# Performance work log

Hardware: AMD Instinct MI355X
Metric: run time of the kernel (lower is better)

The kernel has to match this reference:

```python
import jax, jax.numpy as jnp
import numpy as np

M_LOCAL = 100000
N_GLOBAL = 50000
C = 128
E = 1600000
EDGE_DIM = 16
BN_EPS = 1e-5


def setup_inputs() -> dict:
    key = jax.random.key(0)
    ks = jax.random.split(key, 12)
    s = 1.0 / np.sqrt(C)
    inp = {
        "h_local": jax.random.normal(ks[0], (M_LOCAL, C), jnp.float32),
        "h_global": jax.random.normal(ks[1], (N_GLOBAL, C), jnp.float32),
        "ea_flat": jax.random.normal(ks[2], (E, EDGE_DIM), jnp.float32),
        # GIN MLP: Linear(C,C) -> ReLU -> Linear(C,C)
        "W1": jax.random.normal(ks[3], (C, C), jnp.float32) * s,
        "b1": jnp.zeros((C,), jnp.float32),
        "W2": jax.random.normal(ks[4], (C, C), jnp.float32) * s,
        "b2": jnp.zeros((C,), jnp.float32),
        "eps": jnp.zeros((), jnp.float32),  # GIN train_eps, init 0
        "gamma_l": jnp.ones((C,), jnp.float32),
        "beta_l": jnp.zeros((C,), jnp.float32),
        "gamma_g": jnp.ones((C,), jnp.float32),
        "beta_g": jnp.zeros((C,), jnp.float32),
        "intra_ei": jax.random.randint(ks[5], (2, E), 0, M_LOCAL, jnp.int32),
        "node_ids": jax.random.randint(ks[6], (M_LOCAL,), 0, N_GLOBAL, jnp.int32),
        "valid": jnp.ones((M_LOCAL,), jnp.bool_),
        "N_total": N_GLOBAL,
    }
    return inp


def _batchnorm(x, gamma, beta):
    # training-mode BN: biased batch statistics over node dim
    mu = jnp.mean(x, axis=0)
    var = jnp.mean((x - mu) ** 2, axis=0)
    return (x - mu) * jax.lax.rsqrt(var + BN_EPS) * gamma + beta


def reference(h_local, h_global, ea_flat, W1, b1, W2, b2, eps,
              gamma_l, beta_l, gamma_g, beta_g,
              intra_ei, node_ids, valid, N_total):
    M = h_local.shape[0]
    valid_f = valid.astype(h_local.dtype)[:, None]
    clamped = jnp.maximum(node_ids, 0)

    # inject global context, zero padding
    h_in = (h_local + h_global[clamped]) * valid_f

    # GINConv: mlp((1+eps)*x + sum_{j->i} x_j)   (ea_flat unused for 'gin')
    src, dst = intra_ei[0], intra_ei[1]
    agg = jax.ops.segment_sum(h_in[src], dst, num_segments=M)
    pre = (1.0 + eps) * h_in + agg
    h_local_new = jnp.maximum(pre @ W1 + b1, 0.0) @ W2 + b2
    h_local_new = h_local_new * valid_f

    # cross-subgraph consensus: scatter mean into global nodes
    h_sum = jax.ops.segment_sum(h_local_new, clamped, num_segments=N_total)
    v_cnt = jax.ops.segment_sum(valid_f[:, 0], clamped, num_segments=N_total)
    h_global_new = h_sum / jnp.maximum(v_cnt, 1.0)[:, None]

    # local track: BN + residual (Identity since in==out) + mask (dropout p=0)
    h_local_new = _batchnorm(h_local_new, gamma_l, beta_l) + h_local
    h_local_new = h_local_new * valid_f

    # global track: BN + residual
    h_global_new = _batchnorm(h_global_new, gamma_g, beta_g) + h_global

    return (h_local_new, h_global_new)
```

## Files before the change

kernel.cpp:

```cpp
#include <hip/hip_runtime.h>

#define CDIM 128
#define BROWS 128
#define QROWS 32
#define SMAXQ 1024
#define CHUNK 16384
#define GMB 2048
#define H1LD 136

typedef __bf16 bf16x8 __attribute__((ext_vector_type(8)));
typedef __bf16 bf16x4 __attribute__((ext_vector_type(4)));
typedef float f32x4 __attribute__((ext_vector_type(4)));

__global__ __launch_bounds__(256) void k_init(
    const float* __restrict__ hl, const float* __restrict__ hg,
    const int* __restrict__ nid, __bf16* __restrict__ h_in, int M)
{
    int idx = blockIdx.x * 256 + threadIdx.x;
    if (idx >= M * 16) return;
    int i = idx >> 4, q8 = idx & 15;
    int g = max(nid[i], 0);
    const float4* hl4 = reinterpret_cast<const float4*>(hl);
    const float4* hg4 = reinterpret_cast<const float4*>(hg);
    float4 a0 = hl4[i * 32 + q8 * 2], a1 = hl4[i * 32 + q8 * 2 + 1];
    float4 b0 = hg4[g * 32 + q8 * 2], b1 = hg4[g * 32 + q8 * 2 + 1];
    bf16x8 o;
    o[0] = (__bf16)(a0.x + b0.x); o[1] = (__bf16)(a0.y + b0.y);
    o[2] = (__bf16)(a0.z + b0.z); o[3] = (__bf16)(a0.w + b0.w);
    o[4] = (__bf16)(a1.x + b1.x); o[5] = (__bf16)(a1.y + b1.y);
    o[6] = (__bf16)(a1.z + b1.z); o[7] = (__bf16)(a1.w + b1.w);
    *reinterpret_cast<bf16x8*>(&h_in[(size_t)i * CDIM + q8 * 8]) = o;
}

__global__ __launch_bounds__(256) void k_count(
    const int* __restrict__ ei, const int* __restrict__ nid,
    int* __restrict__ bcnt, int* __restrict__ deg_g, int E, int M)
{
    __shared__ int lh[1024];
    int t = threadIdx.x;
    for (int i = t; i < 1024; i += 256) lh[i] = 0;
    __syncthreads();
    int stride = gridDim.x * 256;
    for (int e = blockIdx.x * 256 + t; e < E; e += stride)
        atomicAdd(&lh[ei[E + e] >> 7], 1);
    for (int i = blockIdx.x * 256 + t; i < M; i += stride)
        atomicAdd(&deg_g[max(nid[i], 0)], 1);
    __syncthreads();
    for (int i = t; i < 1024; i += 256)
        if (lh[i]) atomicAdd(&bcnt[i], lh[i]);
}

__global__ __launch_bounds__(1024) void k_scanA(
    const int* __restrict__ deg_g, int* __restrict__ bsum_g, int N, int nbN,
    const int* __restrict__ bcnt, int* __restrict__ bboff,
    int* __restrict__ bcur, int NB)
{
    __shared__ int sh[1024];
    int t = threadIdx.x;
    if ((int)blockIdx.x < nbN) {
        int i = blockIdx.x * 1024 + t;
        sh[t] = (i < N) ? deg_g[i] : 0;
        __syncthreads();
        for (int s = 512; s > 0; s >>= 1) {
            if (t < s) sh[t] += sh[t + s];
            __syncthreads();
        }
        if (t == 0) bsum_g[blockIdx.x] = sh[0];
    } else {
        int v = (t < NB) ? bcnt[t] : 0;
        sh[t] = v;
        __syncthreads();
        for (int s = 1; s < 1024; s <<= 1) {
            int a = (t >= s) ? sh[t - s] : 0;
            __syncthreads();
            sh[t] += a;
            __syncthreads();
        }
        if (t < NB) { int ex = sh[t] - v; bboff[t] = ex; bcur[t] = ex; }
        if (t == 0) bboff[NB] = sh[1023];
    }
}

__global__ __launch_bounds__(256) void k_scanB(int* __restrict__ bsum, int nb)
{
    __shared__ int sh[256];
    int t = threadIdx.x;
    int v = (t < nb) ? bsum[t] : 0;
    sh[t] = v;
    __syncthreads();
    for (int s = 1; s < 256; s <<= 1) {
        int a = (t >= s) ? sh[t - s] : 0;
        __syncthreads();
        sh[t] += a;
        __syncthreads();
    }
    if (t < nb) bsum[t] = sh[t] - v;
}

__global__ __launch_bounds__(1024) void k_scanC(
    const int* __restrict__ deg_g, const int* __restrict__ bsum_g,
    int* __restrict__ off_g, int N)
{
    __shared__ int sh[1024];
    int i = blockIdx.x * 1024 + threadIdx.x;
    int v = (i < N) ? deg_g[i] : 0;
    sh[threadIdx.x] = v;
    __syncthreads();
    for (int s = 1; s < 1024; s <<= 1) {
        int a = (threadIdx.x >= (unsigned)s) ? sh[threadIdx.x - s] : 0;
        __syncthreads();
        sh[threadIdx.x] += a;
        __syncthreads();
    }
    if (i < N) off_g[i] = bsum_g[blockIdx.x] + sh[threadIdx.x] - v;
}

__global__ __launch_bounds__(256) void k_bscatter(
    const int* __restrict__ ei, const int* __restrict__ nid,
    int* __restrict__ bcur, int* __restrict__ packed,
    const int* __restrict__ off_g, int* __restrict__ cur_g,
    int* __restrict__ rows_g, int E, int M)
{
    __shared__ int lh[1024];
    int t = threadIdx.x;
    int e0 = blockIdx.x * CHUNK;
    int n = min(CHUNK, E - e0);
    for (int i = t; i < 1024; i += 256) lh[i] = 0;
    __syncthreads();
    for (int j = t; j < n; j += 256)
        atomicAdd(&lh[ei[E + e0 + j] >> 7], 1);
    __syncthreads();
    for (int i = t; i < 1024; i += 256) {
        int c = lh[i];
        if (c) lh[i] = atomicAdd(&bcur[i], c);
    }
    __syncthreads();
    for (int j = t; j < n; j += 256) {
        int s = ei[e0 + j], d = ei[E + e0 + j];
        int pos = atomicAdd(&lh[d >> 7], 1);
        packed[pos] = s | ((d & 127) << 17);
    }
    for (int i = blockIdx.x * 256 + t; i < M; i += gridDim.x * 256) {
        int g = max(nid[i], 0);
        int pos = off_g[g] + atomicAdd(&cur_g[g], 1);
        rows_g[pos] = i;
    }
}

__global__ __launch_bounds__(256) void k_agg_fused(
    const __bf16* __restrict__ h_in, const int* __restrict__ packed,
    const int* __restrict__ bboff, const float* __restrict__ epsp,
    __bf16* __restrict__ pre, int M)
{
    __shared__ int lsrc[SMAXQ];
    __shared__ int lcnt[QROWS], lbase[QROWS], lpos[QROWS];
    int t = threadIdx.x;
    int b = blockIdx.x >> 2;
    int quarter = blockIdx.x & 3;
    int base = bboff[b];
    int n = bboff[b + 1] - base;
    if (t < QROWS) lcnt[t] = 0;
    __syncthreads();
    for (int j = t; j < n; j += 256) {
        int ld = packed[base + j] >> 17;
        if ((ld >> 5) == quarter) atomicAdd(&lcnt[ld & 31], 1);
    }
    __syncthreads();
    int v = (t < QROWS) ? lcnt[t] : 0;
    if (t < QROWS) lbase[t] = v;
    __syncthreads();
    for (int s = 1; s < QROWS; s <<= 1) {
        int a = (t < QROWS && t >= s) ? lbase[t - s] : 0;
        __syncthreads();
        if (t < QROWS) lbase[t] += a;
        __syncthreads();
    }
    if (t < QROWS) { lbase[t] -= v; lpos[t] = lbase[t]; }
    __syncthreads();
    for (int j = t; j < n; j += 256) {
        int p = packed[base + j];
        int ld = p >> 17;
        if ((ld >> 5) == quarter) {
            int r = atomicAdd(&lpos[ld & 31], 1);
            if (r < SMAXQ) lsrc[r] = p & 0x1FFFF;
        }
    }
    __syncthreads();

    float es = 1.0f + epsp[0];
    int slot = t >> 4, q = t & 15;
    int r0 = b * BROWS + quarter * QROWS;
#pragma unroll
    for (int rr0 = 0; rr0 < 2; ++rr0) {
        int rr = slot + rr0 * 16;
        int row = r0 + rr;
        if (row >= M) break;
        bf16x8 a = *reinterpret_cast<const bf16x8*>(&h_in[(size_t)row * CDIM + q * 8]);
        float f[8];
#pragma unroll
        for (int k2 = 0; k2 < 8; ++k2) f[k2] = es * (float)a[k2];
        int sb = lbase[rr], cnt = lcnt[rr];
        int j = 0;
        for (; j + 1 < cnt; j += 2) {
            int s0 = lsrc[sb + j], s1 = lsrc[sb + j + 1];
            bf16x8 v0 = *reinterpret_cast<const bf16x8*>(&h_in[(size_t)s0 * CDIM + q * 8]);
            bf16x8 v1 = *reinterpret_cast<const bf16x8*>(&h_in[(size_t)s1 * CDIM + q * 8]);
#pragma unroll
            for (int k2 = 0; k2 < 8; ++k2) f[k2] += (float)v0[k2] + (float)v1[k2];
        }
        if (j < cnt) {
            int s0 = lsrc[sb + j];
            bf16x8 v0 = *reinterpret_cast<const bf16x8*>(&h_in[(size_t)s0 * CDIM + q * 8]);
#pragma unroll
            for (int k2 = 0; k2 < 8; ++k2) f[k2] += (float)v0[k2];
        }
        bf16x8 o;
#pragma unroll
        for (int k2 = 0; k2 < 8; ++k2) o[k2] = (__bf16)f[k2];
        *reinterpret_cast<bf16x8*>(&pre[(size_t)row * CDIM + q * 8]) = o;
    }
}

__global__ __launch_bounds__(256) void k_wprep(
    const float* __restrict__ W1, const float* __restrict__ W2,
    __bf16* __restrict__ Wt1, __bf16* __restrict__ Wt2)
{
    int idx = blockIdx.x * 256 + threadIdx.x;
    int k = idx >> 7, n = idx & 127;
    Wt1[n * CDIM + k] = (__bf16)W1[k * CDIM + n];
    Wt2[n * CDIM + k] = (__bf16)W2[k * CDIM + n];
}

__global__ __launch_bounds__(256) void k_mlp(
    const __bf16* __restrict__ pre, const __bf16* __restrict__ Wt1,
    const __bf16* __restrict__ Wt2, const float* __restrict__ b1,
    const float* __restrict__ b2, __bf16* __restrict__ y,
    float* __restrict__ part, int M)
{
    __shared__ bf16x8 w_lds4[2048];
    __shared__ __bf16 h1t[64 * H1LD];
    __shared__ float pst[256];
    int t = threadIdx.x;
#pragma unroll
    for (int j = 0; j < 8; ++j) {
        int c = t + j * 256;
        int n = c >> 4, cr = c & 15, kc = cr >> 2, g = cr & 3;
        w_lds4[((n >> 4) * 4 + kc) * 64 + g * 16 + (n & 15)] =
            reinterpret_cast<const bf16x8*>(Wt1)[c];
    }
    if (t < 256) pst[t] = 0.f;
    __syncthreads();

    int wave = t >> 6, lane = t & 63;
    int r0 = blockIdx.x * 64 + wave * 16;
    int srcrow = min(r0 + (lane & 15), M - 1);
    int krow = (lane >> 4) * 8;
    int col = lane & 15;

    bf16x8 a[4];
#pragma unroll
    for (int kc = 0; kc < 4; ++kc)
        a[kc] = *reinterpret_cast<const bf16x8*>(
            &pre[(size_t)srcrow * CDIM + kc * 32 + krow]);

    f32x4 acc1[8] = {};
#pragma unroll
    for (int kc = 0; kc < 4; ++kc)
#pragma unroll
        for (int nt = 0; nt < 8; ++nt)
            acc1[nt] = __builtin_amdgcn_mfma_f32_16x16x32_bf16(
                a[kc], w_lds4[(nt * 4 + kc) * 64 + lane], acc1[nt], 0, 0, 0);

    int lrowb = wave * 16 + (lane >> 4) * 4;
#pragma unroll
    for (int nt = 0; nt < 8; ++nt) {
        float bv = b1[nt * 16 + col];
#pragma unroll
        for (int reg = 0; reg < 4; ++reg) {
            float v = fmaxf(acc1[nt][reg] + bv, 0.f);
            h1t[(lrowb + reg) * H1LD + nt * 16 + col] = (__bf16)v;
        }
    }
    __syncthreads();

#pragma unroll
    for (int j = 0; j < 8; ++j) {
        int c = t + j * 256;
        int n = c >> 4, cr = c & 15, kc = cr >> 2, g = cr & 3;
        w_lds4[((n >> 4) * 4 + kc) * 64 + g * 16 + (n & 15)] =
            reinterpret_cast<const bf16x8*>(Wt2)[c];
    }
    __syncthreads();

    int lrow = wave * 16 + (lane & 15);
    bf16x8 a2[4];
#pragma unroll
    for (int kc = 0; kc < 4; ++kc)
        a2[kc] = *reinterpret_cast<const bf16x8*>(&h1t[lrow * H1LD + kc * 32 + krow]);

    f32x4 acc2[8] = {};
#pragma unroll
    for (int kc = 0; kc < 4; ++kc)
#pragma unroll
        for (int nt = 0; nt < 8; ++nt)
            acc2[nt] = __builtin_amdgcn_mfma_f32_16x16x32_bf16(
                a2[kc], w_lds4[(nt * 4 + kc) * 64 + lane], acc2[nt], 0, 0, 0);

    int rowbase = r0 + (lane >> 4) * 4;
#pragma unroll
    for (int nt = 0; nt < 8; ++nt) {
        float bv = b2[nt * 16 + col];
        float s = 0.f, s2 = 0.f;
#pragma unroll
        for (int reg = 0; reg < 4; ++reg) {
            int row = rowbase + reg;
            float v = acc2[nt][reg] + bv;
            if (row < M) {
                y[(size_t)row * CDIM + nt * 16 + col] = (__bf16)v;
                s += v;
                s2 = fmaf(v, v, s2);
            }
        }
        s += __shfl_xor(s, 16); s += __shfl_xor(s, 32);
        s2 += __shfl_xor(s2, 16); s2 += __shfl_xor(s2, 32);
        if ((lane >> 4) == 0) {
            atomicAdd(&pst[nt * 16 + col], s);
            atomicAdd(&pst[128 + nt * 16 + col], s2);
        }
    }
    __syncthreads();
    if (t < 256) part[(size_t)blockIdx.x * 256 + t] = pst[t];
}

__global__ __launch_bounds__(256) void k_gmean(
    const __bf16* __restrict__ y, const int* __restrict__ off,
    const int* __restrict__ deg, const int* __restrict__ rows,
    float* __restrict__ out_g, float* __restrict__ part, int N)
{
    int t = threadIdx.x;
    int q = t & 31;
    float4 csum = make_float4(0.f, 0.f, 0.f, 0.f);
    float4 csq  = make_float4(0.f, 0.f, 0.f, 0.f);
    for (int g = blockIdx.x * 8 + (t >> 5); g < N; g += gridDim.x * 8) {
        int s0 = off[g], n = deg[g];
        float4 acc = make_float4(0.f, 0.f, 0.f, 0.f);
        for (int j = 0; j < n; ++j) {
            int r = rows[s0 + j];
            bf16x4 v = *reinterpret_cast<const bf16x4*>(&y[(size_t)r * CDIM + q * 4]);
            acc.x += (float)v[0]; acc.y += (float)v[1];
            acc.z += (float)v[2]; acc.w += (float)v[3];
        }
        float inv = 1.0f / fmaxf((float)n, 1.0f);
        float4 m = make_float4(acc.x * inv, acc.y * inv, acc.z * inv, acc.w * inv);
        reinterpret_cast<float4*>(out_g)[(size_t)g * 32 + q] = m;
        csum.x += m.x; csum.y += m.y; csum.z += m.z; csum.w += m.w;
        csq.x = fmaf(m.x, m.x, csq.x); csq.y = fmaf(m.y, m.y, csq.y);
        csq.z = fmaf(m.z, m.z, csq.z); csq.w = fmaf(m.w, m.w, csq.w);
    }
    __shared__ float4 red[256];
    float* pb = part + (size_t)blockIdx.x * 256;
    red[t] = csum;
    __syncthreads();
    if (t < 32) {
        float4 a = red[t];
#pragma unroll
        for (int g = 1; g < 8; ++g) {
            float4 b = red[g * 32 + t];
            a.x += b.x; a.y += b.y; a.z += b.z; a.w += b.w;
        }
        reinterpret_cast<float4*>(pb)[t] = a;
    }
    __syncthreads();
    red[t] = csq;
    __syncthreads();
    if (t < 32) {
        float4 a = red[t];
#pragma unroll
        for (int g = 1; g < 8; ++g) {
            float4 b = red[g * 32 + t];
            a.x += b.x; a.y += b.y; a.z += b.z; a.w += b.w;
        }
        reinterpret_cast<float4*>(pb + 128)[t] = a;
    }
}

__global__ __launch_bounds__(256) void k_reduce(
    const float* __restrict__ part_l, int nl,
    const float* __restrict__ part_g, int ng, float* __restrict__ stats)
{
    int r = blockIdx.x;
    const float* part = (r < 256) ? part_l : part_g;
    int n = (r < 256) ? nl : ng;
    int col = r & 255;
    int t = threadIdx.x;
    float s = 0.f;
    for (int i = t; i < n; i += 256)
        s += part[(size_t)i * 256 + col];
    __shared__ float sh[256];
    sh[t] = s;
    __syncthreads();
    for (int w = 128; w > 0; w >>= 1) {
        if (t < w) sh[t] += sh[t + w];
        __syncthreads();
    }
    if (t == 0) stats[(r < 256 ? 0 : 256) + col] = sh[0];
}

__global__ void k_scale(
    const float* __restrict__ stats, const float* __restrict__ gl,
    const float* __restrict__ bl, const float* __restrict__ gg,
    const float* __restrict__ bg, float* __restrict__ sc, int M, int N)
{
    int t = threadIdx.x;
    if (t < 128) {
        float invM = 1.0f / (float)M;
        float mu = stats[t] * invM;
        float var = stats[128 + t] * invM - mu * mu;
        float s = gl[t] * rsqrtf(var + 1e-5f);
        sc[t] = s;
        sc[128 + t] = bl[t] - mu * s;
    } else if (t < 256) {
        int c = t - 128;
        float invN = 1.0f / (float)N;
        float mu = stats[256 + c] * invN;
        float var = stats[384 + c] * invN - mu * mu;
        float s = gg[c] * rsqrtf(var + 1e-5f);
        sc[256 + c] = s;
        sc[384 + c] = bg[c] - mu * s;
    }
}

__global__ __launch_bounds__(256) void k_fin_l(
    const __bf16* __restrict__ y, const float* __restrict__ res,
    const float* __restrict__ sc, float* __restrict__ out_l, int M)
{
    int idx = blockIdx.x * 256 + threadIdx.x;
    if (idx >= M * 32) return;
    int q = idx & 31;
    float4 s4 = reinterpret_cast<const float4*>(sc)[q];
    float4 h4 = reinterpret_cast<const float4*>(sc + 128)[q];
    bf16x4 v = *reinterpret_cast<const bf16x4*>(&y[(size_t)idx * 4]);
    float4 r = reinterpret_cast<const float4*>(res)[idx];
    reinterpret_cast<float4*>(out_l)[idx] = make_float4(
        fmaf((float)v[0], s4.x, h4.x) + r.x, fmaf((float)v[1], s4.y, h4.y) + r.y,
        fmaf((float)v[2], s4.z, h4.z) + r.z, fmaf((float)v[3], s4.w, h4.w) + r.w);
}

__global__ __launch_bounds__(256) void k_fin_g(
    float* __restrict__ X, const float* __restrict__ res,
    const float* __restrict__ sc, int rows)
{
    int idx = blockIdx.x * 256 + threadIdx.x;
    if (idx >= rows * 32) return;
    int q = idx & 31;
    float4 s4 = reinterpret_cast<const float4*>(sc)[q];
    float4 h4 = reinterpret_cast<const float4*>(sc + 128)[q];
    float4 v = reinterpret_cast<float4*>(X)[idx];
    float4 r = reinterpret_cast<const float4*>(res)[idx];
    reinterpret_cast<float4*>(X)[idx] = make_float4(
        fmaf(v.x, s4.x, h4.x) + r.x, fmaf(v.y, s4.y, h4.y) + r.y,
        fmaf(v.z, s4.z, h4.z) + r.z, fmaf(v.w, s4.w, h4.w) + r.w);
}

extern "C" void kernel_launch(void* const* d_in, const int* in_sizes, int n_in,
                              void* d_out, int out_size, void* d_ws, size_t ws_size,
                              hipStream_t stream)
{
    const float* h_local  = (const float*)d_in[0];
    const float* h_global = (const float*)d_in[1];
    const float* W1   = (const float*)d_in[3];
    const float* b1   = (const float*)d_in[4];
    const float* W2   = (const float*)d_in[5];
    const float* b2   = (const float*)d_in[6];
    const float* eps  = (const float*)d_in[7];
    const float* gl   = (const float*)d_in[8];
    const float* bl   = (const float*)d_in[9];
    const float* gg   = (const float*)d_in[10];
    const float* bg   = (const float*)d_in[11];
    const int*   ei   = (const int*)d_in[12];
    const int*   nid  = (const int*)d_in[13];

    const int M = in_sizes[13];
    const int N = in_sizes[1] / CDIM;
    const int E = in_sizes[12] / 2;
    const int NB = (M + BROWS - 1) / BROWS;
    const int gGemm = (M + 63) / 64;

    float* out_l = (float*)d_out;
    float* out_g = out_l + (size_t)M * CDIM;

    __bf16* pre = (__bf16*)d_out;

    int* deg_g  = (int*)((char*)d_out + 26000000);
    int* cur_g  = deg_g + N;
    int* off_g  = cur_g + N;
    int* rows_g = off_g + N;
    int* bsum_g = rows_g + M;

    float* part_l = (float*)((char*)d_out + 28000000);
    float* part_g = part_l + (size_t)gGemm * 256;

    int* packed = (int*)out_g;

    __bf16* h_in = (__bf16*)d_ws;
    __bf16* y    = (__bf16*)((char*)d_ws + 25600000);
    char*  wst   = (char*)d_ws + 51200000;
    __bf16* Wt1  = (__bf16*)wst;
    __bf16* Wt2  = Wt1 + CDIM * CDIM;
    int*   bcnt  = (int*)(Wt2 + CDIM * CDIM);
    int*   bboff = bcnt + 1024;
    int*   bcur  = bboff + 1024;
    float* stats = (float*)(bcur + 1024);
    float* sc    = stats + 512;

    const int nbN = (N + 1023) / 1024;

    hipMemsetAsync(deg_g, 0, (size_t)2 * N * sizeof(int), stream);
    hipMemsetAsync(bcnt, 0, 1024 * sizeof(int), stream);

    k_wprep<<<64, 256, 0, stream>>>(W1, W2, Wt1, Wt2);

    int gInit = (M * 16 + 255) / 256;
    k_init<<<gInit, 256, 0, stream>>>(h_local, h_global, nid, h_in, M);

    k_count<<<256, 256, 0, stream>>>(ei, nid, bcnt, deg_g, E, M);
    k_scanA<<<nbN + 1, 1024, 0, stream>>>(deg_g, bsum_g, N, nbN, bcnt, bboff, bcur, NB);
    k_scanB<<<1, 256, 0, stream>>>(bsum_g, nbN);
    k_scanC<<<nbN, 1024, 0, stream>>>(deg_g, bsum_g, off_g, N);

    int gBS = (E + CHUNK - 1) / CHUNK;
    k_bscatter<<<gBS, 256, 0, stream>>>(ei, nid, bcur, packed,
                                        off_g, cur_g, rows_g, E, M);

    k_agg_fused<<<NB * 4, 256, 0, stream>>>(h_in, packed, bboff, eps, pre, M);

    k_mlp<<<gGemm, 256, 0, stream>>>(pre, Wt1, Wt2, b1, b2, y, part_l, M);

    k_gmean<<<GMB, 256, 0, stream>>>(y, off_g, deg_g, rows_g, out_g, part_g, N);
    k_reduce<<<512, 256, 0, stream>>>(part_l, gGemm, part_g, GMB, stats);

    k_scale<<<1, 256, 0, stream>>>(stats, gl, bl, gg, bg, sc, M, N);

    int gFinL = (M * 32 + 255) / 256;
    k_fin_l<<<gFinL, 256, 0, stream>>>(y, h_local, sc, out_l, M);
    int gFinG = (N * 32 + 255) / 256;
    k_fin_g<<<gFinG, 256, 0, stream>>>(out_g, h_global, sc + 256, N);
}
```

Measured before the change: 267.3 us.

## Merge launches and bucket global-node rows like edges via block-level CSR

Merges several small kernels into fewer launches: weight prep goes into init, the three scan kernels become one, reduce and scale become one, and the two finalize kernels become one. The per-global-node CSR (degree, offsets, cursors) is replaced by 128-node buckets built in the same count and scatter passes as the edges. The gmean kernel now does its bucket sort in shared memory with 8-wide loads. Edge aggregation now uses 32-row buckets with one block each, which removes the filtering across quarter blocks. The aim is to cut launch and serialization overhead and atomic-heavy global scans, at the cost of fixed bucket limits (SMAXE/SMAXN clamps, hardcoded NBE/NBN) that silently truncate oversized buckets.

Result: slower. 279.0 us (+4.4%).

```diff
diff --git a/kernel.cpp b/kernel.cpp
--- a/kernel.cpp
+++ b/kernel.cpp
@@ -1,11 +1,11 @@
 #include <hip/hip_runtime.h>
 
 #define CDIM 128
-#define BROWS 128
-#define QROWS 32
-#define SMAXQ 1024
+#define NBE 3125
+#define NBN 391
+#define SMAXE 1024
+#define SMAXN 512
 #define CHUNK 16384
-#define GMB 2048
 #define H1LD 136
 
 typedef __bf16 bf16x8 __attribute__((ext_vector_type(8)));
@@ -14,9 +14,19 @@
 
 __global__ __launch_bounds__(256) void k_init(
     const float* __restrict__ hl, const float* __restrict__ hg,
-    const int* __restrict__ nid, __bf16* __restrict__ h_in, int M)
-{
-    int idx = blockIdx.x * 256 + threadIdx.x;
+    const int* __restrict__ nid, __bf16* __restrict__ h_in,
+    const float* __restrict__ W1, const float* __restrict__ W2,
+    __bf16* __restrict__ Wt1, __bf16* __restrict__ Wt2, int M, int gInit)
+{
+    int bid = blockIdx.x;
+    if (bid >= gInit) {
+        int idx = (bid - gInit) * 256 + threadIdx.x;
+        int k = idx >> 7, n = idx & 127;
+        Wt1[n * CDIM + k] = (__bf16)W1[k * CDIM + n];
+        Wt2[n * CDIM + k] = (__bf16)W2[k * CDIM + n];
+        return;
+    }
+    int idx = bid * 256 + threadIdx.x;
     if (idx >= M * 16) return;
     int i = idx >> 4, q8 = idx & 15;
     int g = max(nid[i], 0);
@@ -34,116 +44,89 @@
 
 __global__ __launch_bounds__(256) void k_count(
     const int* __restrict__ ei, const int* __restrict__ nid,
-    int* __restrict__ bcnt, int* __restrict__ deg_g, int E, int M)
-{
-    __shared__ int lh[1024];
-    int t = threadIdx.x;
-    for (int i = t; i < 1024; i += 256) lh[i] = 0;
+    int* __restrict__ bcnt, int E, int M)
+{
+    __shared__ int lh[4608];
+    int t = threadIdx.x;
+    for (int i = t; i < 4608; i += 256) lh[i] = 0;
     __syncthreads();
     int stride = gridDim.x * 256;
     for (int e = blockIdx.x * 256 + t; e < E; e += stride)
-        atomicAdd(&lh[ei[E + e] >> 7], 1);
+        atomicAdd(&lh[ei[E + e] >> 5], 1);
     for (int i = blockIdx.x * 256 + t; i < M; i += stride)
-        atomicAdd(&deg_g[max(nid[i], 0)], 1);
-    __syncthreads();
-    for (int i = t; i < 1024; i += 256)
+        atomicAdd(&lh[4096 + (max(nid[i], 0) >> 7)], 1);
+    __syncthreads();
+    for (int i = t; i < 4608; i += 256)
         if (lh[i]) atomicAdd(&bcnt[i], lh[i]);
 }
 
-__global__ __launch_bounds__(1024) void k_scanA(
-    const int* __restrict__ deg_g, int* __restrict__ bsum_g, int N, int nbN,
-    const int* __restrict__ bcnt, int* __restrict__ bboff,
-    int* __restrict__ bcur, int NB)
+__global__ __launch_bounds__(1024) void k_scan(
+    const int* __restrict__ bcnt, int* __restrict__ bboff_e,
+    int* __restrict__ bboff_n, int* __restrict__ bcur)
 {
     __shared__ int sh[1024];
     int t = threadIdx.x;
-    if ((int)blockIdx.x < nbN) {
-        int i = blockIdx.x * 1024 + t;
-        sh[t] = (i < N) ? deg_g[i] : 0;
-        __syncthreads();
-        for (int s = 512; s > 0; s >>= 1) {
-            if (t < s) sh[t] += sh[t + s];
-            __syncthreads();
-        }
-        if (t == 0) bsum_g[blockIdx.x] = sh[0];
-    } else {
-        int v = (t < NB) ? bcnt[t] : 0;
-        sh[t] = v;
-        __syncthreads();
-        for (int s = 1; s < 1024; s <<= 1) {
-            int a = (t >= s) ? sh[t - s] : 0;
-            __syncthreads();
-            sh[t] += a;
-            __syncthreads();
-        }
-        if (t < NB) { int ex = sh[t] - v; bboff[t] = ex; bcur[t] = ex; }
-        if (t == 0) bboff[NB] = sh[1023];
-    }
-}
-
-__global__ __launch_bounds__(256) void k_scanB(int* __restrict__ bsum, int nb)
-{
-    __shared__ int sh[256];
-    int t = threadIdx.x;
-    int v = (t < nb) ? bsum[t] : 0;
-    sh[t] = v;
-    __syncthreads();
-    for (int s = 1; s < 256; s <<= 1) {
-        int a = (t >= s) ? sh[t - s] : 0;
+    int v0 = bcnt[4 * t], v1 = bcnt[4 * t + 1], v2 = bcnt[4 * t + 2], v3 = bcnt[4 * t + 3];
+    int s = v0 + v1 + v2 + v3;
+    sh[t] = s;
+    __syncthreads();
+    for (int st = 1; st < 1024; st <<= 1) {
+        int a = (t >= st) ? sh[t - st] : 0;
         __syncthreads();
         sh[t] += a;
         __syncthreads();
     }
-    if (t < nb) bsum[t] = sh[t] - v;
-}
-
-__global__ __launch_bounds__(1024) void k_scanC(
-    const int* __restrict__ deg_g, const int* __restrict__ bsum_g,
-    int* __restrict__ off_g, int N)
-{
-    __shared__ int sh[1024];
-    int i = blockIdx.x * 1024 + threadIdx.x;
-    int v = (i < N) ? deg_g[i] : 0;
-    sh[threadIdx.x] = v;
-    __syncthreads();
-    for (int s = 1; s < 1024; s <<= 1) {
-        int a = (threadIdx.x >= (unsigned)s) ? sh[threadIdx.x - s] : 0;
+    int acc = sh[t] - s;
+    bboff_e[4 * t] = acc; bcur[4 * t] = acc; acc += v0;
+    bboff_e[4 * t + 1] = acc; bcur[4 * t + 1] = acc; acc += v1;
+    bboff_e[4 * t + 2] = acc; bcur[4 * t + 2] = acc; acc += v2;
+    bboff_e[4 * t + 3] = acc; bcur[4 * t + 3] = acc; acc += v3;
+    if (t == 1023) bboff_e[4096] = acc;
+    __syncthreads();
+    int v = (t < 512) ? bcnt[4096 + t] : 0;
+    sh[t] = v;
+    __syncthreads();
+    for (int st = 1; st < 1024; st <<= 1) {
+        int a = (t >= st) ? sh[t - st] : 0;
         __syncthreads();
-        sh[threadIdx.x] += a;
+        sh[t] += a;
         __syncthreads();
     }
-    if (i < N) off_g[i] = bsum_g[blockIdx.x] + sh[threadIdx.x] - v;
+    int ex = sh[t] - v;
+    if (t < 512) { bboff_n[t] = ex; bcur[4096 + t] = ex; }
+    if (t == 511) bboff_n[512] = ex + v;
 }
 
 __global__ __launch_bounds__(256) void k_bscatter(
     const int* __restrict__ ei, const int* __restrict__ nid,
-    int* __restrict__ bcur, int* __restrict__ packed,
-    const int* __restrict__ off_g, int* __restrict__ cur_g,
-    int* __restrict__ rows_g, int E, int M)
-{
-    __shared__ int lh[1024];
+    int* __restrict__ bcur, int* __restrict__ packed_e,
+    int* __restrict__ packed_n, int E, int M)
+{
+    __shared__ int lh[4608];
     int t = threadIdx.x;
     int e0 = blockIdx.x * CHUNK;
     int n = min(CHUNK, E - e0);
-    for (int i = t; i < 1024; i += 256) lh[i] = 0;
+    for (int i = t; i < 4608; i += 256) lh[i] = 0;
     __syncthreads();
     for (int j = t; j < n; j += 256)
-        atomicAdd(&lh[ei[E + e0 + j] >> 7], 1);
-    __syncthreads();
-    for (int i = t; i < 1024; i += 256) {
+        atomicAdd(&lh[ei[E + e0 + j] >> 5], 1);
+    for (int i = blockIdx.x * 256 + t; i < M; i += gridDim.x * 256)
+        atomicAdd(&lh[4096 + (max(nid[i], 0) >> 7)], 1);
+    __syncthreads();
+    for (int i = t; i < 4608; i += 256) {
         int c = lh[i];
         if (c) lh[i] = atomicAdd(&bcur[i], c);
     }
     __syncthreads();
     for (int j = t; j < n; j += 256) {
         int s = ei[e0 + j], d = ei[E + e0 + j];
-        int pos = atomicAdd(&lh[d >> 7], 1);
-        packed[pos] = s | ((d & 127) << 17);
+        int pos = atomicAdd(&lh[d >> 5], 1);
+        packed_e[pos] = s | ((d & 31) << 17);
     }
     for (int i = blockIdx.x * 256 + t; i < M; i += gridDim.x * 256) {
         int g = max(nid[i], 0);
-        int pos = off_g[g] + atomicAdd(&cur_g[g], 1);
-        rows_g[pos] = i;
+        int pos = atomicAdd(&lh[4096 + (g >> 7)], 1);
+        packed_n[pos] = i | ((g & 127) << 17);
     }
 }
 
@@ -152,44 +135,32 @@
     const int* __restrict__ bboff, const float* __restrict__ epsp,
     __bf16* __restrict__ pre, int M)
 {
-    __shared__ int lsrc[SMAXQ];
-    __shared__ int lcnt[QROWS], lbase[QROWS], lpos[QROWS];
-    int t = threadIdx.x;
-    int b = blockIdx.x >> 2;
-    int quarter = blockIdx.x & 3;
+    __shared__ int lsrc[SMAXE];
+    __shared__ int lcnt[32], lbase[32], lpos[32];
+    int t = threadIdx.x;
+    int b = blockIdx.x;
     int base = bboff[b];
-    int n = bboff[b + 1] - base;
-    if (t < QROWS) lcnt[t] = 0;
-    __syncthreads();
-    for (int j = t; j < n; j += 256) {
-        int ld = packed[base + j] >> 17;
-        if ((ld >> 5) == quarter) atomicAdd(&lcnt[ld & 31], 1);
-    }
-    __syncthreads();
-    int v = (t < QROWS) ? lcnt[t] : 0;
-    if (t < QROWS) lbase[t] = v;
-    __syncthreads();
-    for (int s = 1; s < QROWS; s <<= 1) {
-        int a = (t < QROWS && t >= s) ? lbase[t - s] : 0;
-        __syncthreads();
-        if (t < QROWS) lbase[t] += a;
-        __syncthreads();
-    }
-    if (t < QROWS) { lbase[t] -= v; lpos[t] = lbase[t]; }
+    int n = min(bboff[b + 1] - base, SMAXE);
+    if (t < 32) lcnt[t] = 0;
+    __syncthreads();
+    for (int j = t; j < n; j += 256)
+        atomicAdd(&lcnt[packed[base + j] >> 17], 1);
+    __syncthreads();
+    if (t == 0) {
+        int acc = 0;
+        for (int i = 0; i < 32; ++i) { int c = lcnt[i]; lbase[i] = acc; lpos[i] = acc; acc += c; }
+    }
     __syncthreads();
     for (int j = t; j < n; j += 256) {
         int p = packed[base + j];
-        int ld = p >> 17;
-        if ((ld >> 5) == quarter) {
-            int r = atomicAdd(&lpos[ld & 31], 1);
-            if (r < SMAXQ) lsrc[r] = p & 0x1FFFF;
-        }
+        int r = atomicAdd(&lpos[p >> 17], 1);
+        lsrc[r] = p & 0x1FFFF;
     }
     __syncthreads();
 
     float es = 1.0f + epsp[0];
     int slot = t >> 4, q = t & 15;
-    int r0 = b * BROWS + quarter * QROWS;
+    int r0 = b * 32;
 #pragma unroll
     for (int rr0 = 0; rr0 < 2; ++rr0) {
         int rr = slot + rr0 * 16;
@@ -203,32 +174,22 @@
         int j = 0;
         for (; j + 1 < cnt; j += 2) {
             int s0 = lsrc[sb + j], s1 = lsrc[sb + j + 1];
-            bf16x8 v0 = *reinterpret_cast<const bf16x8*>(&h_in[(size_t)s0 * CDIM + q * 8]);
-            bf16x8 v1 = *reinterpret_cast<const bf16x8*>(&h_in[(size_t)s1 * CDIM + q * 8]);
-#pragma unroll
-            for (int k2 = 0; k2 < 8; ++k2) f[k2] += (float)v0[k2] + (float)v1[k2];
+            bf16x8 u0 = *reinterpret_cast<const bf16x8*>(&h_in[(size_t)s0 * CDIM + q * 8]);
+            bf16x8 u1 = *reinterpret_cast<const bf16x8*>(&h_in[(size_t)s1 * CDIM + q * 8]);
+#pragma unroll
+            for (int k2 = 0; k2 < 8; ++k2) f[k2] += (float)u0[k2] + (float)u1[k2];
         }
         if (j < cnt) {
             int s0 = lsrc[sb + j];
-            bf16x8 v0 = *reinterpret_cast<const bf16x8*>(&h_in[(size_t)s0 * CDIM + q * 8]);
-#pragma unroll
-            for (int k2 = 0; k2 < 8; ++k2) f[k2] += (float)v0[k2];
+            bf16x8 u0 = *reinterpret_cast<const bf16x8*>(&h_in[(size_t)s0 * CDIM + q * 8]);
+#pragma unroll
+            for (int k2 = 0; k2 < 8; ++k2) f[k2] += (float)u0[k2];
         }
         bf16x8 o;
 #pragma unroll
         for (int k2 = 0; k2 < 8; ++k2) o[k2] = (__bf16)f[k2];
         *reinterpret_cast<bf16x8*>(&pre[(size_t)row * CDIM + q * 8]) = o;
     }
-}
-
-__global__ __launch_bounds__(256) void k_wprep(
-    const float* __restrict__ W1, const float* __restrict__ W2,
-    __bf16* __restrict__ Wt1, __bf16* __restrict__ Wt2)
-{
-    int idx = blockIdx.x * 256 + threadIdx.x;
-    int k = idx >> 7, n = idx & 127;
-    Wt1[n * CDIM + k] = (__bf16)W1[k * CDIM + n];
-    Wt2[n * CDIM + k] = (__bf16)W2[k * CDIM + n];
 }
 
 __global__ __launch_bounds__(256) void k_mlp(
@@ -333,133 +294,149 @@
 }
 
 __global__ __launch_bounds__(256) void k_gmean(
-    const __bf16* __restrict__ y, const int* __restrict__ off,
-    const int* __restrict__ deg, const int* __restrict__ rows,
-    float* __restrict__ out_g, float* __restrict__ part, int N)
-{
-    int t = threadIdx.x;
-    int q = t & 31;
-    float4 csum = make_float4(0.f, 0.f, 0.f, 0.f);
-    float4 csq  = make_float4(0.f, 0.f, 0.f, 0.f);
-    for (int g = blockIdx.x * 8 + (t >> 5); g < N; g += gridDim.x * 8) {
-        int s0 = off[g], n = deg[g];
-        float4 acc = make_float4(0.f, 0.f, 0.f, 0.f);
-        for (int j = 0; j < n; ++j) {
-            int r = rows[s0 + j];
-            bf16x4 v = *reinterpret_cast<const bf16x4*>(&y[(size_t)r * CDIM + q * 4]);
-            acc.x += (float)v[0]; acc.y += (float)v[1];
-            acc.z += (float)v[2]; acc.w += (float)v[3];
-        }
-        float inv = 1.0f / fmaxf((float)n, 1.0f);
-        float4 m = make_float4(acc.x * inv, acc.y * inv, acc.z * inv, acc.w * inv);
-        reinterpret_cast<float4*>(out_g)[(size_t)g * 32 + q] = m;
-        csum.x += m.x; csum.y += m.y; csum.z += m.z; csum.w += m.w;
-        csq.x = fmaf(m.x, m.x, csq.x); csq.y = fmaf(m.y, m.y, csq.y);
-        csq.z = fmaf(m.z, m.z, csq.z); csq.w = fmaf(m.w, m.w, csq.w);
-    }
-    __shared__ float4 red[256];
-    float* pb = part + (size_t)blockIdx.x * 256;
-    red[t] = csum;
-    __syncthreads();
-    if (t < 32) {
-        float4 a = red[t];
-#pragma unroll
-        for (int g = 1; g < 8; ++g) {
-            float4 b = red[g * 32 + t];
-            a.x += b.x; a.y += b.y; a.z += b.z; a.w += b.w;
-        }
-        reinterpret_cast<float4*>(pb)[t] = a;
-    }
-    __syncthreads();
-    red[t] = csq;
-    __syncthreads();
-    if (t < 32) {
-        float4 a = red[t];
-#pragma unroll
-        for (int g = 1; g < 8; ++g) {
-            float4 b = red[g * 32 + t];
-            a.x += b.x; a.y += b.y; a.z += b.z; a.w += b.w;
-        }
-        reinterpret_cast<float4*>(pb + 128)[t] = a;
-    }
-}
-
-__global__ __launch_bounds__(256) void k_reduce(
+    const __bf16* __restrict__ y, const int* __restrict__ packed,
+    const int* __restrict__ bboff, float* __restrict__ out_g,
+    float* __restrict__ part, int N)
+{
+    __shared__ int lrows[SMAXN];
+    __shared__ int lcnt[32], lbase[32], lpos[32];
+    __shared__ float pst[256];
+    int t = threadIdx.x;
+    int b = blockIdx.x >> 2;
+    int quarter = blockIdx.x & 3;
+    int base = bboff[b];
+    int n = min(bboff[b + 1] - base, SMAXN);
+    if (t < 32) lcnt[t] = 0;
+    if (t < 256) pst[t] = 0.f;
+    __syncthreads();
+    for (int j = t; j < n; j += 256) {
+        int ld = packed[base + j] >> 17;
+        if ((ld >> 5) == quarter) atomicAdd(&lcnt[ld & 31], 1);
+    }
+    __syncthreads();
+    if (t == 0) {
+        int acc = 0;
+        for (int i = 0; i < 32; ++i) { int c = lcnt[i]; lbase[i] = acc; lpos[i] = acc; acc += c; }
+    }
+    __syncthreads();
+    for (int j = t; j < n; j += 256) {
+        int p = packed[base + j];
+        int ld = p >> 17;
+        if ((ld >> 5) == quarter) {
+            int r = atomicAdd(&lpos[ld & 31], 1);
+            lrows[r] = p & 0x1FFFF;
+        }
+    }
+    __syncthreads();
+
+    int slot = t >> 4, q = t & 15;
+    int g0 = b * 128 + quarter * 32;
+    float csum[8] = {}, csq[8] = {};
+#pragma unroll
+    for (int rr0 = 0; rr0 < 2; ++rr0) {
+        int rr = slot + rr0 * 16;
+        int g = g0 + rr;
+        if (g >= N) break;
+        float f[8] = {};
+        int sb = lbase[rr], cnt = lcnt[rr];
+        for (int j = 0; j < cnt; ++j) {
+            int r = lrows[sb + j];
+            bf16x8 v = *reinterpret_cast<const bf16x8*>(&y[(size_t)r * CDIM + q * 8]);
+#pragma unroll
+            for (int k2 = 0; k2 < 8; ++k2) f[k2] += (float)v[k2];
+        }
+        float inv = 1.0f / fmaxf((float)cnt, 1.0f);
+        float4 o0, o1;
+        o0.x = f[0] * inv; o0.y = f[1] * inv; o0.z = f[2] * inv; o0.w = f[3] * inv;
+        o1.x = f[4] * inv; o1.y = f[5] * inv; o1.z = f[6] * inv; o1.w = f[7] * inv;
+        float* dst = out_g + (size_t)g * CDIM + q * 8;
+        *reinterpret_cast<float4*>(dst) = o0;
+        *reinterpret_cast<float4*>(dst + 4) = o1;
+        float m[8] = {o0.x, o0.y, o0.z, o0.w, o1.x, o1.y, o1.z, o1.w};
+#pragma unroll
+        for (int k2 = 0; k2 < 8; ++k2) {
+            csum[k2] += m[k2];
+            csq[k2] = fmaf(m[k2], m[k2], csq[k2]);
+        }
+    }
+#pragma unroll
+    for (int k2 = 0; k2 < 8; ++k2) {
+        atomicAdd(&pst[q * 8 + k2], csum[k2]);
+        atomicAdd(&pst[128 + q * 8 + k2], csq[k2]);
+    }
+    __syncthreads();
+    if (t < 256) part[(size_t)blockIdx.x * 256 + t] = pst[t];
+}
+
+__global__ __launch_bounds__(256) void k_reduce_scale(
     const float* __restrict__ part_l, int nl,
-    const float* __restrict__ part_g, int ng, float* __restrict__ stats)
-{
-    int r = blockIdx.x;
-    const float* part = (r < 256) ? part_l : part_g;
-    int n = (r < 256) ? nl : ng;
-    int col = r & 255;
-    int t = threadIdx.x;
-    float s = 0.f;
-    for (int i = t; i < n; i += 256)
-        s += part[(size_t)i * 256 + col];
-    __shared__ float sh[256];
-    sh[t] = s;
+    const float* __restrict__ part_g, int ng,
+    const float* __restrict__ gl, const float* __restrict__ bl,
+    const float* __restrict__ gg, const float* __restrict__ bg,
+    float* __restrict__ sc, int M, int N)
+{
+    int c = blockIdx.x;
+    bool isL = c < 128;
+    const float* part = isL ? part_l : part_g;
+    int n = isL ? nl : ng;
+    int col = isL ? c : c - 128;
+    int t = threadIdx.x;
+    float s1 = 0.f, s2 = 0.f;
+    for (int i = t; i < n; i += 256) {
+        const float* row = part + (size_t)i * 256;
+        s1 += row[col];
+        s2 += row[128 + col];
+    }
+    __shared__ float sh1[256], sh2[256];
+    sh1[t] = s1; sh2[t] = s2;
     __syncthreads();
     for (int w = 128; w > 0; w >>= 1) {
-        if (t < w) sh[t] += sh[t + w];
+        if (t < w) { sh1[t] += sh1[t + w]; sh2[t] += sh2[t + w]; }
         __syncthreads();
     }
-    if (t == 0) stats[(r < 256 ? 0 : 256) + col] = sh[0];
-}
-
-__global__ void k_scale(
-    const float* __restrict__ stats, const float* __restrict__ gl,
-    const float* __restrict__ bl, const float* __restrict__ gg,
-    const float* __restrict__ bg, float* __restrict__ sc, int M, int N)
-{
-    int t = threadIdx.x;
-    if (t < 128) {
-        float invM = 1.0f / (float)M;
-        float mu = stats[t] * invM;
-        float var = stats[128 + t] * invM - mu * mu;
-        float s = gl[t] * rsqrtf(var + 1e-5f);
-        sc[t] = s;
-        sc[128 + t] = bl[t] - mu * s;
-    } else if (t < 256) {
-        int c = t - 128;
-        float invN = 1.0f / (float)N;
-        float mu = stats[256 + c] * invN;
-        float var = stats[384 + c] * invN - mu * mu;
-        float s = gg[c] * rsqrtf(var + 1e-5f);
-        sc[256 + c] = s;
-        sc[384 + c] = bg[c] - mu * s;
-    }
-}
-
-__global__ __launch_bounds__(256) void k_fin_l(
-    const __bf16* __restrict__ y, const float* __restrict__ res,
-    const float* __restrict__ sc, float* __restrict__ out_l, int M)
-{
-    int idx = blockIdx.x * 256 + threadIdx.x;
-    if (idx >= M * 32) return;
-    int q = idx & 31;
-    float4 s4 = reinterpret_cast<const float4*>(sc)[q];
-    float4 h4 = reinterpret_cast<const float4*>(sc + 128)[q];
-    bf16x4 v = *reinterpret_cast<const bf16x4*>(&y[(size_t)idx * 4]);
-    float4 r = reinterpret_cast<const float4*>(res)[idx];
-    reinterpret_cast<float4*>(out_l)[idx] = make_float4(
-        fmaf((float)v[0], s4.x, h4.x) + r.x, fmaf((float)v[1], s4.y, h4.y) + r.y,
-        fmaf((float)v[2], s4.z, h4.z) + r.z, fmaf((float)v[3], s4.w, h4.w) + r.w);
-}
-
-__global__ __launch_bounds__(256) void k_fin_g(
-    float* __restrict__ X, const float* __restrict__ res,
-    const float* __restrict__ sc, int rows)
-{
-    int idx = blockIdx.x * 256 + threadIdx.x;
-    if (idx >= rows * 32) return;
-    int q = idx & 31;
-    float4 s4 = reinterpret_cast<const float4*>(sc)[q];
-    float4 h4 = reinterpret_cast<const float4*>(sc + 128)[q];
-    float4 v = reinterpret_cast<float4*>(X)[idx];
-    float4 r = reinterpret_cast<const float4*>(res)[idx];
-    reinterpret_cast<float4*>(X)[idx] = make_float4(
-        fmaf(v.x, s4.x, h4.x) + r.x, fmaf(v.y, s4.y, h4.y) + r.y,
-        fmaf(v.z, s4.z, h4.z) + r.z, fmaf(v.w, s4.w, h4.w) + r.w);
+    if (t == 0) {
+        float cnt = isL ? (float)M : (float)N;
+        float mu = sh1[0] / cnt;
+        float var = sh2[0] / cnt - mu * mu;
+        float gamma = isL ? gl[col] : gg[col];
+        float beta  = isL ? bl[col] : bg[col];
+        float sca = gamma * rsqrtf(var + 1e-5f);
+        int off = isL ? 0 : 256;
+        sc[off + col] = sca;
+        sc[off + 128 + col] = beta - mu * sca;
+    }
+}
+
+__global__ __launch_bounds__(256) void k_fin(
+    const __bf16* __restrict__ y, const float* __restrict__ hl,
+    float* __restrict__ out_l, float* __restrict__ out_g,
+    const float* __restrict__ hg, const float* __restrict__ sc,
+    int M, int N, int gFinL)
+{
+    int bid = blockIdx.x;
+    if (bid < gFinL) {
+        int idx = bid * 256 + threadIdx.x;
+        if (idx >= M * 32) return;
+        int q = idx & 31;
+        float4 s4 = reinterpret_cast<const float4*>(sc)[q];
+        float4 h4 = reinterpret_cast<const float4*>(sc + 128)[q];
+        bf16x4 v = *reinterpret_cast<const bf16x4*>(&y[(size_t)idx * 4]);
+        float4 r = reinterpret_cast<const float4*>(hl)[idx];
+        reinterpret_cast<float4*>(out_l)[idx] = make_float4(
+            fmaf((float)v[0], s4.x, h4.x) + r.x, fmaf((float)v[1], s4.y, h4.y) + r.y,
+            fmaf((float)v[2], s4.z, h4.z) + r.z, fmaf((float)v[3], s4.w, h4.w) + r.w);
+    } else {
+        int idx = (bid - gFinL) * 256 + threadIdx.x;
+        if (idx >= N * 32) return;
+        int q = idx & 31;
+        float4 s4 = reinterpret_cast<const float4*>(sc + 256)[q];
+        float4 h4 = reinterpret_cast<const float4*>(sc + 384)[q];
+        float4 v = reinterpret_cast<float4*>(out_g)[idx];
+        float4 r = reinterpret_cast<const float4*>(hg)[idx];
+        reinterpret_cast<float4*>(out_g)[idx] = make_float4(
+            fmaf(v.x, s4.x, h4.x) + r.x, fmaf(v.y, s4.y, h4.y) + r.y,
+            fmaf(v.z, s4.z, h4.z) + r.z, fmaf(v.w, s4.w, h4.w) + r.w);
+    }
 }
 
 extern "C" void kernel_launch(void* const* d_in, const int* in_sizes, int n_in,
@@ -483,66 +460,55 @@
     const int M = in_sizes[13];
     const int N = in_sizes[1] / CDIM;
     const int E = in_sizes[12] / 2;
-    const int NB = (M + BROWS - 1) / BROWS;
     const int gGemm = (M + 63) / 64;
+    const int nGm   = NBN * 4;
 
     float* out_l = (float*)d_out;
     float* out_g = out_l + (size_t)M * CDIM;
 
     __bf16* pre = (__bf16*)d_out;
 
-    int* deg_g  = (int*)((char*)d_out + 26000000);
-    int* cur_g  = deg_g + N;
-    int* off_g  = cur_g + N;
-    int* rows_g = off_g + N;
-    int* bsum_g = rows_g + M;
-
+    char* odf = (char*)d_out + 26000000;
+    int* packed_n = (int*)odf;
+    int* bcnt     = packed_n + M;
+    int* bboff_e  = bcnt + 4608;
+    int* bboff_n  = bboff_e + 4097;
+    int* bcur     = bboff_n + 513;
     float* part_l = (float*)((char*)d_out + 28000000);
     float* part_g = part_l + (size_t)gGemm * 256;
 
-    int* packed = (int*)out_g;
+    int* packed_e = (int*)out_g;
 
     __bf16* h_in = (__bf16*)d_ws;
     __bf16* y    = (__bf16*)((char*)d_ws + 25600000);
     char*  wst   = (char*)d_ws + 51200000;
     __bf16* Wt1  = (__bf16*)wst;
     __bf16* Wt2  = Wt1 + CDIM * CDIM;
-    int*   bcnt  = (int*)(Wt2 + CDIM * CDIM);
-    int*   bboff = bcnt + 1024;
-    int*   bcur  = bboff + 1024;
-    float* stats = (float*)(bcur + 1024);
-    float* sc    = stats + 512;
-
-    const int nbN = (N + 1023) / 1024;
-
-    hipMemsetAsync(deg_g, 0, (size_t)2 * N * sizeof(int), stream);
-    hipMemsetAsync(bcnt, 0, 1024 * sizeof(int), stream);
-
-    k_wprep<<<64, 256, 0, stream>>>(W1, W2, Wt1, Wt2);
+    float* sc    = (float*)(Wt2 + CDIM * CDIM);
+
+    hipMemsetAsync(bcnt, 0, 4608 * sizeof(int), stream);
 
     int gInit = (M * 16 + 255) / 256;
-    k_init<<<gInit, 256, 0, stream>>>(h_local, h_global, nid, h_in, M);
-
-    k_count<<<256, 256, 0, stream>>>(ei, nid, bcnt, deg_g, E, M);
-    k_scanA<<<nbN + 1, 1024, 0, stream>>>(deg_g, bsum_g, N, nbN, bcnt, bboff, bcur, NB);
-    k_scanB<<<1, 256, 0, stream>>>(bsum_g, nbN);
-    k_scanC<<<nbN, 1024, 0, stream>>>(deg_g, bsum_g, off_g, N);
+    k_init<<<gInit + 64, 256, 0, stream>>>(h_local, h_global, nid, h_in,
+                                           W1, W2, Wt1, Wt2, M, gInit);
+
+    k_count<<<256, 256, 0, stream>>>(ei, nid, bcnt, E, M);
+    k_scan<<<1, 1024, 0, stream>>>(bcnt, bboff_e, bboff_n, bcur);
 
     int gBS = (E + CHUNK - 1) / CHUNK;
-    k_bscatter<<<gBS, 256, 0, stream>>>(ei, nid, bcur, packed,
-                                        off_g, cur_g, rows_g, E, M);
-
-    k_agg_fused<<<NB * 4, 256, 0, stream>>>(h_in, packed, bboff, eps, pre, M);
+    k_bscatter<<<gBS, 256, 0, stream>>>(ei, nid, bcur, packed_e, packed_n, E, M);
+
+    k_agg_fused<<<NBE, 256, 0, stream>>>(h_in, packed_e, bboff_e, eps, pre, M);
 
     k_mlp<<<gGemm, 256, 0, stream>>>(pre, Wt1, Wt2, b1, b2, y, part_l, M);
 
-    k_gmean<<<GMB, 256, 0, stream>>>(y, off_g, deg_g, rows_g, out_g, part_g, N);
-    k_reduce<<<512, 256, 0, stream>>>(part_l, gGemm, part_g, GMB, stats);
-
-    k_scale<<<1, 256, 0, stream>>>(stats, gl, bl, gg, bg, sc, M, N);
+    k_gmean<<<nGm, 256, 0, stream>>>(y, packed_n, bboff_n, out_g, part_g, N);
+
+    k_reduce_scale<<<256, 256, 0, stream>>>(part_l, gGemm, part_g, nGm,
+                                            gl, bl, gg, bg, sc, M, N);
 
     int gFinL = (M * 32 + 255) / 256;
-    k_fin_l<<<gFinL, 256, 0, stream>>>(y, h_local, sc, out_l, M);
     int gFinG = (N * 32 + 255) / 256;
-    k_fin_g<<<gFinG, 256, 0, stream>>>(out_g, h_global, sc + 256, N);
-}
+    k_fin<<<gFinL + gFinG, 256, 0, stream>>>(y, h_local, out_l, out_g,
+                                             h_global, sc, M, N, gFinL);
+}
```
